# Kernel tuning notes

Hardware: AMD Instinct MI355X
Metric: run time of the kernel (lower is better)

The kernel has to match this reference:

```python
import jax, jax.numpy as jnp
import numpy as np

HEAD_DIM = 64
NUM_HEADS = 32
ROPE_THETA = 10000.0


def _rope_cos_sin(seq_len, dim, theta, dtype):
    inv_freq = 1.0 / (theta ** (jnp.arange(0, dim, 2, dtype=jnp.float32) / dim))
    t = jnp.arange(seq_len, dtype=jnp.float32)
    freqs = jnp.outer(t, inv_freq)  # [T, dim/2]
    return jnp.cos(freqs).astype(dtype), jnp.sin(freqs).astype(dtype)


def _apply_rope(x, cos, sin):
    # x: [B, T, H, D]; GPT-NeoX style (split halves), matching flash-attn rotary (interleaved=False)
    d2 = x.shape[-1] // 2
    x1, x2 = x[..., :d2], x[..., d2:]
    c = cos[None, :, None, :]
    s = sin[None, :, None, :]
    return jnp.concatenate([x1 * c - x2 * s, x2 * c + x1 * s], axis=-1)


def setup_inputs() -> dict:
    key = jax.random.key(0)
    ks = jax.random.split(key, 8)
    B, T, Dm = 2, 2048, 2048
    H, Dh = NUM_HEADS, HEAD_DIM
    sc = 1.0 / np.sqrt(Dm)
    return {
        "hidden_states": jax.random.normal(ks[0], (B, T, Dm), jnp.float32),
        "v1": jax.random.normal(ks[1], (B, T, H, Dh), jnp.float32),
        "lambda1": jax.random.uniform(ks[2], (), jnp.float32),
        "Wq": jax.random.normal(ks[3], (Dm, Dm), jnp.float32) * sc,
        "Wk": jax.random.normal(ks[4], (Dm, Dm), jnp.float32) * sc,
        "Wv": jax.random.normal(ks[5], (Dm, Dm), jnp.float32) * sc,
        "Wo": jax.random.normal(ks[6], (Dm, Dm), jnp.float32) * sc,
        "lambda2": jnp.float32(0.5),
    }


def reference(hidden_states, v1, lambda1, Wq, Wk, Wv, Wo, lambda2):
    B, T, Dm = hidden_states.shape
    H, Dh = NUM_HEADS, HEAD_DIM
    # QKV projections + head split
    q = (hidden_states @ Wq).reshape(B, T, H, Dh)
    k = (hidden_states @ Wk).reshape(B, T, H, Dh)
    v = (hidden_states @ Wv).reshape(B, T, H, Dh)
    # Value residual mixing: V' = lambda1 * V_1 + lambda2 * V_n
    v = lambda1 * v1 + lambda2 * v
    # RoPE (seqlen_offset = 0, no cache)
    cos, sin = _rope_cos_sin(T, Dh, ROPE_THETA, q.dtype)
    q = _apply_rope(q, cos, sin)
    k = _apply_rope(k, cos, sin)
    # Causal attention (flash_attn_func(..., causal=True) equivalent)
    scale = 1.0 / np.sqrt(Dh)
    scores = jnp.einsum("bqhd,bkhd->bhqk", q, k) * scale
    causal = jnp.tril(jnp.ones((T, T), dtype=bool))
    scores = jnp.where(causal[None, None], scores, jnp.finfo(scores.dtype).min)
    probs = jax.nn.softmax(scores, axis=-1)
    o = jnp.einsum("bhqk,bkhd->bqhd", probs, v).reshape(B, T, Dm)
    return o @ Wo
```

## Files before the change

kernel.cpp:

```cpp
#include <hip/hip_runtime.h>
#include <hip/hip_bf16.h>
#include <math.h>

typedef __bf16 bf16;
typedef __bf16 bf16x8 __attribute__((ext_vector_type(8)));
typedef __bf16 bf16x4 __attribute__((ext_vector_type(4)));
typedef float  f32x4  __attribute__((ext_vector_type(4)));
typedef short  sv4    __attribute__((ext_vector_type(4)));

#define B_  2
#define T_  2048
#define DM  2048
#define H_  32
#define DH  64

__device__ __forceinline__ bf16x8 load8(const bf16* p) {
    return *reinterpret_cast<const bf16x8*>(p);
}

__device__ __forceinline__ void gld16(const bf16* g, bf16* l) {
    __builtin_amdgcn_global_load_lds(
        (const __attribute__((address_space(1))) unsigned int*)g,
        (__attribute__((address_space(3))) unsigned int*)l, 16, 0, 0);
}

__global__ void k_convert(const float* __restrict__ in, bf16* __restrict__ out, int n4) {
    int i = blockIdx.x * blockDim.x + threadIdx.x;
    if (i < n4) {
        float4 v = reinterpret_cast<const float4*>(in)[i];
        bf16x4 o;
        o[0] = (bf16)v.x; o[1] = (bf16)v.y; o[2] = (bf16)v.z; o[3] = (bf16)v.w;
        reinterpret_cast<bf16x4*>(out)[i] = o;
    }
}

__global__ void k_transposeW(const float* __restrict__ Wq, const float* __restrict__ Wk,
                             const float* __restrict__ Wv, const float* __restrict__ Wo,
                             bf16* __restrict__ WqT, bf16* __restrict__ WkT,
                             bf16* __restrict__ WvT, bf16* __restrict__ WoT) {
    const float* in; bf16* out;
    switch (blockIdx.z) {
        case 0: in = Wq; out = WqT; break;
        case 1: in = Wk; out = WkT; break;
        case 2: in = Wv; out = WvT; break;
        default: in = Wo; out = WoT; break;
    }
    __shared__ float tile[32][33];
    int tx = threadIdx.x, ty = threadIdx.y;
    int x0 = blockIdx.x * 32, y0 = blockIdx.y * 32;
    #pragma unroll
    for (int i = 0; i < 4; i++)
        tile[ty + i*8][tx] = in[(size_t)(y0 + ty + i*8) * DM + x0 + tx];
    __syncthreads();
    #pragma unroll
    for (int i = 0; i < 4; i++)
        out[(size_t)(x0 + ty + i*8) * DM + y0 + tx] = (bf16)tile[tx][ty + i*8];
}

template<int OUT_BF16>
__global__ __launch_bounds__(256)
void k_gemm(const bf16* __restrict__ A, const bf16* __restrict__ BT,
            void* __restrict__ Cout, int ldc) {
    constexpr int K = 2048;
    __shared__ bf16 ldsA[128 * 32];
    __shared__ bf16 ldsB[128 * 32];
    int tid = threadIdx.x;
    int lane = tid & 63, w = tid >> 6;
    int l16 = lane & 15, quad = lane >> 4;
    int wm = w >> 1, wn = w & 1;
    int mblk = blockIdx.y * 128, nblk = blockIdx.x * 128;

    f32x4 acc[4][4] = {};

    int sgz = ((lane & 3) ^ ((lane >> 3) & 3)) * 8;
    const bf16* gA = A  + (size_t)(mblk + w * 32 + (lane >> 2)) * K + sgz;
    const bf16* gB = BT + (size_t)(nblk + w * 32 + (lane >> 2)) * K + sgz;
    bf16* lA = ldsA + w * 1024;
    bf16* lB = ldsB + w * 1024;
    int sA = (quad ^ ((l16 >> 1) & 3)) * 8;

    for (int k0 = 0; k0 < K; k0 += 32) {
        gld16(gA + k0,          lA);
        gld16(gA + 16 * K + k0, lA + 512);
        gld16(gB + k0,          lB);
        gld16(gB + 16 * K + k0, lB + 512);
        __syncthreads();
        bf16x8 af[4], bfr[4];
        #pragma unroll
        for (int s = 0; s < 4; s++)
            af[s] = *reinterpret_cast<bf16x8*>(&ldsA[(wm * 64 + s * 16 + l16) * 32 + sA]);
        #pragma unroll
        for (int t = 0; t < 4; t++)
            bfr[t] = *reinterpret_cast<bf16x8*>(&ldsB[(wn * 64 + t * 16 + l16) * 32 + sA]);
        #pragma unroll
        for (int s = 0; s < 4; s++)
            #pragma unroll
            for (int t = 0; t < 4; t++)
                acc[s][t] = __builtin_amdgcn_mfma_f32_16x16x32_bf16(af[s], bfr[t], acc[s][t], 0, 0, 0);
        __syncthreads();
    }

    #pragma unroll
    for (int s = 0; s < 4; s++) {
        int row = mblk + wm * 64 + s * 16 + quad * 4;
        #pragma unroll
        for (int t = 0; t < 4; t++) {
            int col = nblk + wn * 64 + t * 16 + l16;
            #pragma unroll
            for (int r = 0; r < 4; r++) {
                if (OUT_BF16)
                    reinterpret_cast<bf16*>(Cout)[(size_t)(row + r) * ldc + col] = (bf16)acc[s][t][r];
                else
                    reinterpret_cast<float*>(Cout)[(size_t)(row + r) * ldc + col] = acc[s][t][r];
            }
        }
    }
}

template<int OUT_BF16>
__global__ __launch_bounds__(512, 2)
void k_gemm256(const bf16* __restrict__ A, const bf16* __restrict__ BT,
               void* __restrict__ Cout, int ldc) {
    constexpr int K = 2048;
    __shared__ bf16 lds[32768];
    const int tid  = threadIdx.x;
    const int lane = tid & 63, w = tid >> 6;
    const int l16  = lane & 15, quad = lane >> 4;
    const int wm   = w >> 2, wn = w & 3;
    const size_t mblk = (size_t)blockIdx.y * 256, nblk = (size_t)blockIdx.x * 256;

    f32x4 acc[8][4] = {};

    const int sg = (((tid & 3) ^ ((tid >> 3) & 3)) << 3);
    const bf16* gA = A  + (mblk + (tid >> 2)) * K + sg;
    const bf16* gB = BT + (nblk + (tid >> 2)) * K + sg;

    const int segr = ((quad ^ ((l16 >> 1) & 3)) << 3);
    const int aoff = (wm * 128 + l16) * 32 + segr;
    const int boff = (wn * 64  + l16) * 32 + segr;

#define STGA(kt_) do { \
    const bf16* g_ = gA + (kt_) * 32; \
    bf16* l_ = lds + ((((kt_) & 1) << 14) + 8192) + w * 512; \
    gld16(g_, l_); gld16(g_ + 128 * 2048, l_ + 4096); \
} while (0)

#define STGB(kt_) do { \
    const bf16* g_ = gB + (kt_) * 32; \
    bf16* l_ = lds + (((kt_) & 1) << 14) + w * 512; \
    gld16(g_, l_); gld16(g_ + 128 * 2048, l_ + 4096); \
} while (0)

#define LD4(dst_, base_) do { \
    _Pragma("unroll") for (int i_ = 0; i_ < 4; ++i_) \
        dst_[i_] = *reinterpret_cast<const bf16x8*>((base_) + i_ * 512); \
} while (0)

#define MFMA16(mh_) do { \
    _Pragma("unroll") for (int mi_ = 0; mi_ < 4; ++mi_) \
        _Pragma("unroll") for (int ni_ = 0; ni_ < 4; ++ni_) \
            acc[(mh_) * 4 + mi_][ni_] = __builtin_amdgcn_mfma_f32_16x16x32_bf16( \
                af[mi_], bq[ni_], acc[(mh_) * 4 + mi_][ni_], 0, 0, 0); \
} while (0)

#define BAR  __builtin_amdgcn_s_barrier()
#define PRI1 __builtin_amdgcn_s_setprio(1)
#define PRI0 __builtin_amdgcn_s_setprio(0)
#define VM2  asm volatile("s_waitcnt vmcnt(2)" ::: "memory")
#define VM0  asm volatile("s_waitcnt vmcnt(0)" ::: "memory")

#define TILE(cb_, S0_, S1_, VM_) do { \
    const bf16* rb_ = lds + (cb_) + boff; \
    const bf16* ra_ = lds + (cb_) + 8192 + aoff; \
    bf16x8 af[4], bq[4]; \
    LD4(af, ra_); LD4(bq, rb_); \
    S0_; BAR; PRI1; MFMA16(0); PRI0; BAR; \
    LD4(af, ra_ + 2048); \
    S1_; BAR; PRI1; MFMA16(1); PRI0; VM_; BAR; \
} while (0)

    STGB(0); STGA(0); STGB(1);
    VM2;
    BAR;

    #pragma unroll 1
    for (int t = 0; t < 61; t += 2) {
        TILE(0,     STGA(t + 1), STGB(t + 2), VM2);
        TILE(16384, STGA(t + 2), STGB(t + 3), VM2);
    }
    TILE(0,     STGA(63), (void)0, VM0);
    TILE(16384, (void)0, (void)0, (void)0);

#undef STGA
#undef STGB
#undef LD4
#undef MFMA16
#undef BAR
#undef PRI1
#undef PRI0
#undef VM2
#undef VM0
#undef TILE

    #pragma unroll
    for (int mt = 0; mt < 8; ++mt) {
        size_t row = mblk + wm * 128 + mt * 16 + quad * 4;
        #pragma unroll
        for (int nt = 0; nt < 4; ++nt) {
            size_t col = nblk + wn * 64 + nt * 16 + l16;
            #pragma unroll
            for (int r = 0; r < 4; ++r) {
                if (OUT_BF16)
                    reinterpret_cast<bf16*>(Cout)[(row + r) * (size_t)ldc + col] = (bf16)acc[mt][nt][r];
                else
                    reinterpret_cast<float*>(Cout)[(row + r) * (size_t)ldc + col] = acc[mt][nt][r];
            }
        }
    }
}

__global__ void k_tab(float2* __restrict__ tab) {
    int id = blockIdx.x * 256 + threadIdx.x;
    int i = id & 31, t = id >> 5;
    float inv = __builtin_amdgcn_exp2f(-(float)i * 0.41524101186092037f);
    float ang = (float)t * inv;
    float s, c;
    __sincosf(ang, &s, &c);
    tab[id] = make_float2(c, s);
}

__global__ void k_rope(bf16* __restrict__ qkv, const float2* __restrict__ tab) {
    int id = blockIdx.x * 256 + threadIdx.x;
    int j   = id & 3;
    int h   = (id >> 2) & 31;
    int sel = (id >> 7) & 1;
    int t   = (id >> 8) & 2047;
    int b   = id >> 19;
    size_t base = ((size_t)(b * T_ + t)) * 6144 + sel * 2048 + h * 64 + j * 8;
    bf16x8 x1 = load8(qkv + base);
    bf16x8 x2 = load8(qkv + base + 32);
    const float2* tp = tab + t * 32 + j * 8;
    bf16x8 o1, o2;
    #pragma unroll
    for (int e = 0; e < 8; e++) {
        float c = tp[e].x, s = tp[e].y;
        float a = (float)x1[e], v = (float)x2[e];
        o1[e] = (bf16)(a * c - v * s);
        o2[e] = (bf16)(v * c + a * s);
    }
    *reinterpret_cast<bf16x8*>(qkv + base)      = o1;
    *reinterpret_cast<bf16x8*>(qkv + base + 32) = o2;
}

__global__ void k_combinev(const float* __restrict__ v1, const bf16* __restrict__ qkv,
                           const float* __restrict__ l1p, const float* __restrict__ l2p,
                           bf16* __restrict__ vT) {
    __shared__ float tile[64 * 33];
    float l1 = l1p[0], l2 = l2p[0];
    int b = blockIdx.y >> 5, h = blockIdx.y & 31;
    int t0 = blockIdx.x * 32;
    int tid = threadIdx.x;
    int d = tid & 63, tr = tid >> 6;
    #pragma unroll
    for (int i = 0; i < 8; i++) {
        int t = t0 + i * 4 + tr;
        size_t iv1 = ((size_t)(b * T_ + t)) * 2048 + h * 64 + d;
        size_t ivg = ((size_t)(b * T_ + t)) * 6144 + 4096 + h * 64 + d;
        tile[d * 33 + i * 4 + tr] = l1 * v1[iv1] + l2 * (float)qkv[ivg];
    }
    __syncthreads();
    int tl = tid & 31, dr = tid >> 5;
    #pragma unroll
    for (int j = 0; j < 8; j++) {
        int d2 = dr + j * 8;
        vT[((size_t)((b * H_ + h) * 64 + d2)) * T_ + t0 + tl] = (bf16)tile[d2 * 33 + tl];
    }
}

__global__ __launch_bounds__(256)
void k_attn(const bf16* __restrict__ qkv, const bf16* __restrict__ vT, bf16* __restrict__ o) {
    __shared__ bf16 ldsK[64 * 64];
    __shared__ bf16 ldsV[64 * 64];
    int bx = blockIdx.x;
    int bh = blockIdx.y;
    int b = bh >> 5, h = bh & 31;
    int tid = threadIdx.x;
    int lane = tid & 63, w = tid >> 6;
    int l16 = lane & 15, quad = lane >> 4;

    int rl = lane >> 3, sg = ((lane & 7) ^ rl) * 8;
    const bf16* kgl = qkv + ((size_t)(b * T_) + w * 16 + rl) * 6144 + 2048 + h * 64 + sg;
    const bf16* vgl = vT + ((size_t)bh * DH + w * 16 + rl) * T_ + sg;
    bf16* lKw = ldsK + w * 16 * 64;
    bf16* lVw = ldsV + w * 16 * 64;

    int skey = (quad ^ (l16 & 7)) * 8;
    int skey2 = ((quad + 4) ^ (l16 & 7)) * 8;

    #pragma unroll 1
    for (int pass = 0; pass < 2; pass++) {
        int qt = pass ? (31 - bx) : bx;
        int qbase = qt * 64 + w * 16;

        size_t qrow = (size_t)(b * T_ + qbase + l16) * 6144 + h * 64;
        bf16x8 qf[2];
        #pragma unroll
        for (int half = 0; half < 2; half++) {
            bf16x8 v = load8(qkv + qrow + half * 32 + quad * 8);
            #pragma unroll
            for (int e = 0; e < 8; e++) v[e] = (bf16)((float)v[e] * 0.1803368801f);
            qf[half] = v;
        }

        f32x4 accO[4] = {};
        float m_ = -1e30f, pl = 0.f;

        int nkt = qt + 1;
        for (int kt = 0; kt < nkt; kt++) {
            int key0 = kt * 64;
            #pragma unroll
            for (int j = 0; j < 2; j++) {
                gld16(kgl + (size_t)(key0 + j * 8) * 6144, lKw + j * 512);
                gld16(vgl + (size_t)(j * 8) * T_ + key0,   lVw + j * 512);
            }
            __syncthreads();

            bool diag = (kt == qt);
            f32x4 st[4];
            sv4 pk[4];
            #pragma unroll
            for (int ks = 0; ks < 4; ks++) {
                if (!diag || key0 + ks * 16 <= qbase + 15) {
                    bf16x8 kf0 = *reinterpret_cast<bf16x8*>(&ldsK[(ks * 16 + l16) * 64 + skey]);
                    bf16x8 kf1 = *reinterpret_cast<bf16x8*>(&ldsK[(ks * 16 + l16) * 64 + skey2]);
                    f32x4 z = {};
                    z = __builtin_amdgcn_mfma_f32_16x16x32_bf16(kf0, qf[0], z, 0, 0, 0);
                    z = __builtin_amdgcn_mfma_f32_16x16x32_bf16(kf1, qf[1], z, 0, 0, 0);
                    st[ks] = z;
                } else {
                    st[ks] = (f32x4){-3e38f, -3e38f, -3e38f, -3e38f};
                }
            }

            if (diag) {
                int qcol = qbase + l16;
                #pragma unroll
                for (int ks = 0; ks < 4; ks++)
                    #pragma unroll
                    for (int r = 0; r < 4; r++)
                        if (key0 + ks * 16 + quad * 4 + r > qcol) st[ks][r] = -3e38f;
            }

            float mx = st[0][0];
            #pragma unroll
            for (int ks = 0; ks < 4; ks++)
                #pragma unroll
                for (int r = 0; r < 4; r++) mx = fmaxf(mx, st[ks][r]);
            mx = fmaxf(mx, __shfl_xor(mx, 16));
            mx = fmaxf(mx, __shfl_xor(mx, 32));
            if (__any(mx > m_)) {
                float nm = fmaxf(m_, mx);
                float alpha = __builtin_amdgcn_exp2f(m_ - nm);
                m_ = nm;
                pl *= alpha;
                #pragma unroll
                for (int n2 = 0; n2 < 4; n2++) accO[n2] *= alpha;
            }
            float rsum = 0.f;
            #pragma unroll
            for (int ks = 0; ks < 4; ks++) {
                bf16x4 ph;
                #pragma unroll
                for (int r = 0; r < 4; r++) {
                    float p = __builtin_amdgcn_exp2f(st[ks][r] - m_);
                    rsum += p;
                    ph[r] = (bf16)p;
                }
                pk[ks] = __builtin_bit_cast(sv4, ph);
            }
            pl += rsum;

            #pragma unroll
            for (int ks = 0; ks < 4; ks++) {
                if (!diag || key0 + ks * 16 <= qbase + 15) {
                    int svf = ((ks * 2 + (quad >> 1)) ^ (l16 & 7)) * 8 + (quad & 1) * 4;
                    #pragma unroll
                    for (int n2 = 0; n2 < 4; n2++) {
                        sv4 vf = *reinterpret_cast<sv4*>(&ldsV[(n2 * 16 + l16) * 64 + svf]);
                        accO[n2] = __builtin_amdgcn_mfma_f32_16x16x16bf16_1k(
                            vf, pk[ks], accO[n2], 0, 0, 0);
                    }
                }
            }
            __syncthreads();
        }

        float l = pl;
        l += __shfl_xor(l, 16);
        l += __shfl_xor(l, 32);
        float inv = 1.0f / l;
        int query = qbase + l16;
        #pragma unroll
        for (int n2 = 0; n2 < 4; n2++) {
            bf16x4 ov;
            #pragma unroll
            for (int r = 0; r < 4; r++) ov[r] = (bf16)(accO[n2][r] * inv);
            *reinterpret_cast<bf16x4*>(
                &o[(size_t)(b * T_ + query) * DM + h * 64 + n2 * 16 + quad * 4]) = ov;
        }
    }
}

extern "C" void kernel_launch(void* const* d_in, const int* in_sizes, int n_in,
                              void* d_out, int out_size, void* d_ws, size_t ws_size,
                              hipStream_t stream) {
    const float* hs   = (const float*)d_in[0];
    const float* v1   = (const float*)d_in[1];
    const float* lam1 = (const float*)d_in[2];
    const float* Wq   = (const float*)d_in[3];
    const float* Wk   = (const float*)d_in[4];
    const float* Wv   = (const float*)d_in[5];
    const float* Wo   = (const float*)d_in[6];
    const float* lam2 = (const float*)d_in[7];

    char* ws = (char*)d_ws;
    bf16* hs_bf = (bf16*)(ws);
    float2* tab = (float2*)(ws);
    bf16* Wcat  = (bf16*)(ws + 16777216);
    bf16* WoT   = (bf16*)(ws + 41943040);
    bf16* qkv   = (bf16*)(ws + 50331648);
    bf16* vT_bf = (bf16*)(ws + 100663296);
    bf16* o_bf  = (bf16*)(ws + 117440512);

    k_convert<<<8192, 256, 0, stream>>>(hs, hs_bf, 2097152);
    k_transposeW<<<dim3(64, 64, 4), dim3(32, 8), 0, stream>>>(
        Wq, Wk, Wv, Wo, Wcat, Wcat + 4194304, Wcat + 8388608, WoT);

    k_gemm256<1><<<dim3(24, 16), 512, 0, stream>>>(hs_bf, Wcat, (void*)qkv, 6144);

    k_tab<<<256, 256, 0, stream>>>(tab);
    k_rope<<<4096, 256, 0, stream>>>(qkv, tab);

    k_combinev<<<dim3(64, 64), 256, 0, stream>>>(v1, qkv, lam1, lam2, vT_bf);

    k_attn<<<dim3(16, 64), 256, 0, stream>>>(qkv, vT_bf, o_bf);

    k_gemm<0><<<dim3(16, 32), 256, 0, stream>>>(o_bf, WoT, d_out, 2048);
}
```

Measured before the change: 442.0 us.

## Restructure GEMM main loop to prefetch full tiles with fewer barriers

The GEMM inner loop now reads all eight A fragments and the B fragments from LDS up front. It waits on lgkmcnt once, then takes a single barrier before issuing global-to-LDS loads for both A and B of tile t+2 into the buffer just consumed. This halves the per-tile barrier count, and the prologue stages two full tiles with a vmcnt(4) wait. The aim is to cut synchronization stalls and let MFMA work overlap with prefetch. The cost is more VGPRs for the fragments, which may lower occupancy.

After: 440.0 us. About the same (-0.5%).

```diff
diff --git a/kernel.cpp b/kernel.cpp
--- a/kernel.cpp
+++ b/kernel.cpp
@@ -151,44 +151,52 @@
     gld16(g_, l_); gld16(g_ + 128 * 2048, l_ + 4096); \
 } while (0)
 
-#define LD4(dst_, base_) do { \
+#define LD4(dst_, i0_, base_) do { \
     _Pragma("unroll") for (int i_ = 0; i_ < 4; ++i_) \
-        dst_[i_] = *reinterpret_cast<const bf16x8*>((base_) + i_ * 512); \
+        dst_[(i0_) + i_] = *reinterpret_cast<const bf16x8*>((base_) + i_ * 512); \
 } while (0)
 
 #define MFMA16(mh_) do { \
     _Pragma("unroll") for (int mi_ = 0; mi_ < 4; ++mi_) \
         _Pragma("unroll") for (int ni_ = 0; ni_ < 4; ++ni_) \
             acc[(mh_) * 4 + mi_][ni_] = __builtin_amdgcn_mfma_f32_16x16x32_bf16( \
-                af[mi_], bq[ni_], acc[(mh_) * 4 + mi_][ni_], 0, 0, 0); \
+                af[(mh_) * 4 + mi_], bq[ni_], acc[(mh_) * 4 + mi_][ni_], 0, 0, 0); \
 } while (0)
 
 #define BAR  __builtin_amdgcn_s_barrier()
 #define PRI1 __builtin_amdgcn_s_setprio(1)
 #define PRI0 __builtin_amdgcn_s_setprio(0)
-#define VM2  asm volatile("s_waitcnt vmcnt(2)" ::: "memory")
+#define LGK0 asm volatile("s_waitcnt lgkmcnt(0)" ::: "memory")
+#define VM4  asm volatile("s_waitcnt vmcnt(4)" ::: "memory")
 #define VM0  asm volatile("s_waitcnt vmcnt(0)" ::: "memory")
 
-#define TILE(cb_, S0_, S1_, VM_) do { \
+#define TILE(cb_, SA_, SB_, VM_) do { \
     const bf16* rb_ = lds + (cb_) + boff; \
     const bf16* ra_ = lds + (cb_) + 8192 + aoff; \
-    bf16x8 af[4], bq[4]; \
-    LD4(af, ra_); LD4(bq, rb_); \
-    S0_; BAR; PRI1; MFMA16(0); PRI0; BAR; \
-    LD4(af, ra_ + 2048); \
-    S1_; BAR; PRI1; MFMA16(1); PRI0; VM_; BAR; \
+    bf16x8 af[8], bq[4]; \
+    LD4(af, 0, ra_); \
+    LD4(af, 4, ra_ + 2048); \
+    LD4(bq, 0, rb_); \
+    LGK0; \
+    BAR; \
+    SA_; \
+    PRI1; MFMA16(0); PRI0; \
+    SB_; \
+    PRI1; MFMA16(1); PRI0; \
+    VM_; \
+    BAR; \
 } while (0)
 
-    STGB(0); STGA(0); STGB(1);
-    VM2;
+    STGB(0); STGA(0); STGB(1); STGA(1);
+    VM4;
     BAR;
 
     #pragma unroll 1
     for (int t = 0; t < 61; t += 2) {
-        TILE(0,     STGA(t + 1), STGB(t + 2), VM2);
-        TILE(16384, STGA(t + 2), STGB(t + 3), VM2);
-    }
-    TILE(0,     STGA(63), (void)0, VM0);
+        TILE(0,     STGA(t + 2), STGB(t + 2), VM4);
+        TILE(16384, STGA(t + 3), STGB(t + 3), VM4);
+    }
+    TILE(0,     (void)0, (void)0, VM0);
     TILE(16384, (void)0, (void)0, (void)0);
 
 #undef STGA
@@ -198,7 +206,8 @@
 #undef BAR
 #undef PRI1
 #undef PRI0
-#undef VM2
+#undef LGK0
+#undef VM4
 #undef VM0
 #undef TILE
 
```
